# Performance work log

Hardware: AMD Instinct MI355X
Metric: run time of the kernel (lower is better)

## Reference

```python
import jax, jax.numpy as jnp
import numpy as np

T, XDIM, ZDIM = 500000, 64, 64


def setup_inputs() -> dict:
    key = jax.random.key(0)
    ks = jax.random.split(key, 6)
    return {
        "X_t": jax.random.normal(ks[0], (T, XDIM), dtype=jnp.float32),
        "Z_t": jax.random.normal(ks[1], (T, ZDIM), dtype=jnp.float32),
        "G": jax.random.uniform(ks[2], (), dtype=jnp.float32),
        "eta": jax.random.normal(ks[3], (XDIM,), dtype=jnp.float32),
        "zeta": jax.random.normal(ks[4], (ZDIM,), dtype=jnp.float32),
        "gamma": jax.random.normal(ks[5], (ZDIM,), dtype=jnp.float32),
    }


def reference(X_t, Z_t, G, eta, zeta, gamma):
    # theta_t = sigmoid(G) * theta_{t-1} + dot(Z[t-1], gamma), theta_0 = 0
    # Y_t = theta_t + dot(X[t], eta) + dot(Z[t], zeta)
    G_hat = jax.nn.sigmoid(G)  # addSigmoid=True path
    c = Z_t @ gamma                                   # [T]
    u = jnp.concatenate([jnp.zeros((1,), c.dtype), c[:-1]])  # shifted drive, u_0 = 0
    a = jnp.full_like(u, G_hat)

    def combine(x, y):
        a1, b1 = x
        a2, b2 = y
        return a1 * a2, b1 * a2 + b2

    _, theta = jax.lax.associative_scan(combine, (a, u))  # [T], theta_0 = 0
    return theta + X_t @ eta + Z_t @ zeta
```

## Files before the change

kernel.cpp:

```cpp
#include <hip/hip_runtime.h>


#define WIN     64
#define CHUNK   128
#define P2C     256
#define FCHUNK  256
#define RPI     64
#define NITER   ((WIN + FCHUNK) / RPI)

template <int N>
__device__ __forceinline__ float rshr_add(float v) {
    const int s = __builtin_amdgcn_update_dpp(
        0, __float_as_int(v), 0x110 | N , 0xF, 0xF, true);
    return v + __int_as_float(s);
}
__device__ __forceinline__ float rsum16(float v) {
    v = rshr_add<8>(v);
    v = rshr_add<4>(v);
    v = rshr_add<2>(v);
    v = rshr_add<1>(v);
    return v;
}

__device__ __forceinline__ void gload16(const float* g, float* l) {
    __builtin_amdgcn_global_load_lds(
        (const __attribute__((address_space(1))) void*)g,
        (__attribute__((address_space(3))) void*)l, 16, 0, 0);
}

__global__ __launch_bounds__(256) void dlm_pass1(
    const float* __restrict__ X, const float* __restrict__ Z,
    const float* __restrict__ eta, const float* __restrict__ zeta,
    const float* __restrict__ gam,
    float* __restrict__ c_ws, float* __restrict__ b_out, int T)
{
    const int tid  = threadIdx.x;
    const int lane = tid & 63;
    const int wv   = tid >> 6;
    const int sub  = lane & 15;
    const int rsub = lane >> 4;
    const int s    = (int)blockIdx.x * CHUNK;
    const int Tm1  = T - 1;

    __shared__ __align__(16) float zl[CHUNK * 64];
    __shared__ __align__(16) float xl[CHUNK * 64];

    const float4 e4  = ((const float4*)eta)[sub];
    const float4 sz4 = ((const float4*)zeta)[sub];
    const float4 g4  = ((const float4*)gam)[sub];

    #pragma unroll
    for (int j = 0; j < 8; ++j) {
        const int rb = wv * 32 + j * 4;
        const int r  = rb + (lane >> 4);
        const int gr = min(s + r, Tm1);
        const int gs = (lane & 15) ^ (r & 7);
        const size_t o = (size_t)gr * 64 + gs * 4;
        gload16(Z + o, &zl[rb * 64]);
        gload16(X + o, &xl[rb * 64]);
    }
    asm volatile("s_waitcnt vmcnt(0)" ::: "memory");
    __syncthreads();

    #pragma unroll
    for (int i = 0; i < CHUNK / 64; ++i) {
        #pragma unroll
        for (int u = 0; u < 4; ++u) {
            const int ri = i * 64 + wv * 16 + u * 4 + rsub;
            const int sl = ((sub ^ (ri & 7)) << 2);
            const float4 z = *(const float4*)&zl[ri * 64 + sl];
            const float4 x = *(const float4*)&xl[ri * 64 + sl];
            float cp = z.x*g4.x + z.y*g4.y + z.z*g4.z + z.w*g4.w;
            float bp = x.x*e4.x + x.y*e4.y + x.z*e4.z + x.w*e4.w
                     + z.x*sz4.x + z.y*sz4.y + z.z*sz4.z + z.w*sz4.w;
            cp = rsum16(cp);
            bp = rsum16(bp);
            const int t = s + ri;
            if (sub == 15 && t < T) {
                c_ws[t]  = cp;
                b_out[t] = bp;
            }
        }
    }
}

__global__ __launch_bounds__(256) void dlm_pass2(
    const float* __restrict__ c, const float* __restrict__ Gp,
    float* __restrict__ out, int T)
{
    const int tid = threadIdx.x;
    const int s   = (int)blockIdx.x * P2C;
    const int t   = s + tid;

    __shared__ float sc[P2C];
    __shared__ float theta_sh;

    const float g   = *Gp;
    const float a   = 1.0f / (1.0f + expf(-g));
    const float l2a = log2f(a);

    const float v = (t >= 1 && t < T) ? c[t - 1] : 0.0f;
    const float b = (t < T) ? out[t] : 0.0f;

    if (tid < 64) {
        float term = 0.0f;
        const int idx = s - 2 - tid;
        if (tid <= WIN - 2 && idx >= 0)
            term = exp2f((float)tid * l2a) * c[idx];
        #pragma unroll
        for (int off = 1; off <= 32; off <<= 1)
            term += __shfl_xor(term, off, 64);
        if (tid == 0) theta_sh = term;
    }

    sc[tid] = v;
    __syncthreads();
    const float theta_in = theta_sh;

    float Ad = a;
    for (int d = 1; d < P2C; d <<= 1) {
        const float self = sc[tid];
        const float prev = (tid >= d) ? sc[tid - d] : 0.0f;
        __syncthreads();
        sc[tid] = self + Ad * prev;
        __syncthreads();
        Ad *= Ad;
    }

    const float E = (tid > 0) ? sc[tid - 1] : 0.0f;
    float theta = exp2f((float)tid * l2a) * theta_in + E;
    theta = a * theta + v;
    if (t < T) out[t] = b + theta;
}

__global__ __launch_bounds__(256) void dlm_fused(
    const float* __restrict__ X, const float* __restrict__ Z,
    const float* __restrict__ Gp,
    const float* __restrict__ eta, const float* __restrict__ zeta,
    const float* __restrict__ gam,
    float* __restrict__ out, int T)
{
    const int tid  = threadIdx.x;
    const int lane = tid & 63;
    const int wv   = tid >> 6;
    const int sub  = lane & 15;
    const int rsub = lane >> 4;
    const int s    = (int)blockIdx.x * FCHUNK;

    __shared__ float cl[WIN + FCHUNK];
    __shared__ float bl[FCHUNK];
    __shared__ float sc[256];
    __shared__ float theta_sh;

    const float4 e4  = ((const float4*)eta)[sub];
    const float4 sz4 = ((const float4*)zeta)[sub];
    const float4 g4  = ((const float4*)gam)[sub];
    const float4* X4 = (const float4*)X;
    const float4* Z4 = (const float4*)Z;

    const float g   = *Gp;
    const float a   = 1.0f / (1.0f + expf(-g));
    const float l2a = log2f(a);

    for (int i = 0; i < NITER; ++i) {
        const int rb = s - WIN + i * RPI + wv * 16;
        float cp[4], bp[4];
        #pragma unroll
        for (int u = 0; u < 4; ++u) {
            const int r = rb + u * 4 + rsub;
            float4 z = make_float4(0.f, 0.f, 0.f, 0.f);
            float4 x = make_float4(0.f, 0.f, 0.f, 0.f);
            const bool in = (r >= 0) && (r < T);
            if (in)           z = Z4[(size_t)r * 16 + sub];
            if (in && i > 0)  x = X4[(size_t)r * 16 + sub];
            cp[u] = z.x*g4.x + z.y*g4.y + z.z*g4.z + z.w*g4.w;
            bp[u] = x.x*e4.x + x.y*e4.y + x.z*e4.z + x.w*e4.w
                  + z.x*sz4.x + z.y*sz4.y + z.z*sz4.z + z.w*sz4.w;
        }
        #pragma unroll
        for (int u = 0; u < 4; ++u) {
            #pragma unroll
            for (int off = 1; off <= 8; off <<= 1) {
                cp[u] += __shfl_xor(cp[u], off, 64);
                bp[u] += __shfl_xor(bp[u], off, 64);
            }
        }
        if (sub == 0) {
            #pragma unroll
            for (int u = 0; u < 4; ++u) {
                const int r = rb + u * 4 + rsub;
                cl[r - s + WIN] = cp[u];
                if (i > 0) bl[r - s] = bp[u];
            }
        }
    }
    __syncthreads();

    if (tid < 64) {
        float term = 0.0f;
        if (tid <= WIN - 2)
            term = exp2f((float)tid * l2a) * cl[WIN - 2 - tid];
        #pragma unroll
        for (int off = 1; off <= 32; off <<= 1)
            term += __shfl_xor(term, off, 64);
        if (tid == 0) theta_sh = term;
    }

    const int t = s + tid;
    const float v = (t == 0) ? 0.0f : cl[WIN + tid - 1];
    sc[tid] = v;
    __syncthreads();
    const float theta_in = theta_sh;

    float Ad = a;
    for (int d = 1; d < 256; d <<= 1) {
        const float self = sc[tid];
        const float prev = (tid >= d) ? sc[tid - d] : 0.0f;
        __syncthreads();
        sc[tid] = self + Ad * prev;
        __syncthreads();
        Ad *= Ad;
    }

    const float E = (tid > 0) ? sc[tid - 1] : 0.0f;
    float theta = exp2f((float)tid * l2a) * theta_in + E;
    theta = a * theta + v;
    if (t < T) out[t] = bl[tid] + theta;
}

extern "C" void kernel_launch(void* const* d_in, const int* in_sizes, int n_in,
                              void* d_out, int out_size, void* d_ws, size_t ws_size,
                              hipStream_t stream) {
    const float* X     = (const float*)d_in[0];
    const float* Z     = (const float*)d_in[1];
    const float* G     = (const float*)d_in[2];
    const float* eta   = (const float*)d_in[3];
    const float* zeta  = (const float*)d_in[4];
    const float* gamma = (const float*)d_in[5];
    float* out = (float*)d_out;

    const int T = in_sizes[0] / 64;

    if (ws_size >= (size_t)T * sizeof(float)) {
        float* c_ws = (float*)d_ws;
        const int nb1 = (T + CHUNK - 1) / CHUNK;
        const int nb2 = (T + P2C - 1) / P2C;
        dlm_pass1<<<nb1, 256, 0, stream>>>(X, Z, eta, zeta, gamma, c_ws, out, T);
        dlm_pass2<<<nb2, 256, 0, stream>>>(c_ws, G, out, T);
    } else {
        const int nbf = (T + FCHUNK - 1) / FCHUNK;
        dlm_fused<<<nbf, 256, 0, stream>>>(X, Z, G, eta, zeta, gamma, out, T);
    }
}
```

Before: 277.3 us.

## Split pass1 into separate Z and X streaming kernels with register double-buffering

```diff
diff --git a/kernel.cpp b/kernel.cpp
--- a/kernel.cpp
+++ b/kernel.cpp
@@ -2,7 +2,7 @@
 
 
 #define WIN     64
-#define CHUNK   128
+#define CHUNK   256
 #define P2C     256
 #define FCHUNK  256
 #define RPI     64
@@ -22,17 +22,10 @@
     return v;
 }
 
-__device__ __forceinline__ void gload16(const float* g, float* l) {
-    __builtin_amdgcn_global_load_lds(
-        (const __attribute__((address_space(1))) void*)g,
-        (__attribute__((address_space(3))) void*)l, 16, 0, 0);
-}
-
-__global__ __launch_bounds__(256) void dlm_pass1(
-    const float* __restrict__ X, const float* __restrict__ Z,
-    const float* __restrict__ eta, const float* __restrict__ zeta,
-    const float* __restrict__ gam,
-    float* __restrict__ c_ws, float* __restrict__ b_out, int T)
+__global__ __launch_bounds__(256) void dlm_zpass(
+    const float* __restrict__ Z,
+    const float* __restrict__ zeta, const float* __restrict__ gam,
+    float* __restrict__ c_ws, float* __restrict__ out, int T)
 {
     const int tid  = threadIdx.x;
     const int lane = tid & 63;
@@ -42,46 +35,101 @@
     const int s    = (int)blockIdx.x * CHUNK;
     const int Tm1  = T - 1;
 
-    __shared__ __align__(16) float zl[CHUNK * 64];
-    __shared__ __align__(16) float xl[CHUNK * 64];
-
-    const float4 e4  = ((const float4*)eta)[sub];
     const float4 sz4 = ((const float4*)zeta)[sub];
     const float4 g4  = ((const float4*)gam)[sub];
-
-    #pragma unroll
-    for (int j = 0; j < 8; ++j) {
-        const int rb = wv * 32 + j * 4;
-        const int r  = rb + (lane >> 4);
-        const int gr = min(s + r, Tm1);
-        const int gs = (lane & 15) ^ (r & 7);
-        const size_t o = (size_t)gr * 64 + gs * 4;
-        gload16(Z + o, &zl[rb * 64]);
-        gload16(X + o, &xl[rb * 64]);
-    }
-    asm volatile("s_waitcnt vmcnt(0)" ::: "memory");
-    __syncthreads();
-
-    #pragma unroll
-    for (int i = 0; i < CHUNK / 64; ++i) {
-        #pragma unroll
-        for (int u = 0; u < 4; ++u) {
-            const int ri = i * 64 + wv * 16 + u * 4 + rsub;
-            const int sl = ((sub ^ (ri & 7)) << 2);
-            const float4 z = *(const float4*)&zl[ri * 64 + sl];
-            const float4 x = *(const float4*)&xl[ri * 64 + sl];
-            float cp = z.x*g4.x + z.y*g4.y + z.z*g4.z + z.w*g4.w;
-            float bp = x.x*e4.x + x.y*e4.y + x.z*e4.z + x.w*e4.w
-                     + z.x*sz4.x + z.y*sz4.y + z.z*sz4.z + z.w*sz4.w;
-            cp = rsum16(cp);
-            bp = rsum16(bp);
-            const int t = s + ri;
-            if (sub == 15 && t < T) {
-                c_ws[t]  = cp;
-                b_out[t] = bp;
+    const float4* Z4 = (const float4*)Z;
+
+    float4 A[4], B[4];
+
+    auto issue = [&](float4 (&buf)[4], int i) {
+        const int rb = s + i * 64 + wv * 16;
+        #pragma unroll
+        for (int u = 0; u < 4; ++u) {
+            const int r = min(rb + u * 4 + rsub, Tm1);
+            buf[u] = Z4[(size_t)r * 16 + sub];
+        }
+    };
+
+    auto reduce_store = [&](const float4 (&buf)[4], int i) {
+        float cp[4], zp[4];
+        #pragma unroll
+        for (int u = 0; u < 4; ++u) {
+            const float4 z = buf[u];
+            cp[u] = z.x*g4.x + z.y*g4.y + z.z*g4.z + z.w*g4.w;
+            zp[u] = z.x*sz4.x + z.y*sz4.y + z.z*sz4.z + z.w*sz4.w;
+            cp[u] = rsum16(cp[u]);
+            zp[u] = rsum16(zp[u]);
+        }
+        if (sub == 15) {
+            #pragma unroll
+            for (int u = 0; u < 4; ++u) {
+                const int t = s + i * 64 + wv * 16 + u * 4 + rsub;
+                if (t < T) { c_ws[t] = cp[u]; out[t] = zp[u]; }
             }
         }
-    }
+    };
+
+    issue(A, 0);
+    issue(B, 1);
+    reduce_store(A, 0);
+    issue(A, 2);
+    reduce_store(B, 1);
+    issue(B, 3);
+    reduce_store(A, 2);
+    reduce_store(B, 3);
+}
+
+__global__ __launch_bounds__(256) void dlm_xpass(
+    const float* __restrict__ X, const float* __restrict__ eta,
+    float* __restrict__ out, int T)
+{
+    const int tid  = threadIdx.x;
+    const int lane = tid & 63;
+    const int wv   = tid >> 6;
+    const int sub  = lane & 15;
+    const int rsub = lane >> 4;
+    const int s    = (int)blockIdx.x * CHUNK;
+    const int Tm1  = T - 1;
+
+    const float4 e4  = ((const float4*)eta)[sub];
+    const float4* X4 = (const float4*)X;
+
+    float4 A[4], B[4];
+
+    auto issue = [&](float4 (&buf)[4], int i) {
+        const int rb = s + i * 64 + wv * 16;
+        #pragma unroll
+        for (int u = 0; u < 4; ++u) {
+            const int r = min(rb + u * 4 + rsub, Tm1);
+            buf[u] = X4[(size_t)r * 16 + sub];
+        }
+    };
+
+    auto reduce_store = [&](const float4 (&buf)[4], int i) {
+        float xp[4];
+        #pragma unroll
+        for (int u = 0; u < 4; ++u) {
+            const float4 x = buf[u];
+            xp[u] = x.x*e4.x + x.y*e4.y + x.z*e4.z + x.w*e4.w;
+            xp[u] = rsum16(xp[u]);
+        }
+        if (sub == 15) {
+            #pragma unroll
+            for (int u = 0; u < 4; ++u) {
+                const int t = s + i * 64 + wv * 16 + u * 4 + rsub;
+                if (t < T) out[t] += xp[u];
+            }
+        }
+    };
+
+    issue(A, 0);
+    issue(B, 1);
+    reduce_store(A, 0);
+    issue(A, 2);
+    reduce_store(B, 1);
+    issue(B, 3);
+    reduce_store(A, 2);
+    reduce_store(B, 3);
 }
 
 __global__ __launch_bounds__(256) void dlm_pass2(
@@ -243,9 +291,10 @@
 
     if (ws_size >= (size_t)T * sizeof(float)) {
         float* c_ws = (float*)d_ws;
-        const int nb1 = (T + CHUNK - 1) / CHUNK;
+        const int nb  = (T + CHUNK - 1) / CHUNK;
         const int nb2 = (T + P2C - 1) / P2C;
-        dlm_pass1<<<nb1, 256, 0, stream>>>(X, Z, eta, zeta, gamma, c_ws, out, T);
+        dlm_zpass<<<nb, 256, 0, stream>>>(Z, zeta, gamma, c_ws, out, T);
+        dlm_xpass<<<nb, 256, 0, stream>>>(X, eta, out, T);
         dlm_pass2<<<nb2, 256, 0, stream>>>(c_ws, G, out, T);
     } else {
         const int nbf = (T + FCHUNK - 1) / FCHUNK;
```

New measurement: 282.1 us. About the same (+1.8%).
